# Performance work log

Measured on AMD Instinct MI355X. Metric: run time of the kernel, lower is better.

Reference implementation:

```python
import jax, jax.numpy as jnp
import numpy as np

# Model dims (match init_kwargs)
N_HEADS = 32
N_KV_HEADS = 8
DIM = 4096
HEAD_DIM = DIM // N_HEADS  # 128
N_REP = N_HEADS // N_KV_HEADS  # 4
MAX_SEQ_LEN = 2048
THETA = 10000.0


def precompute_freqs(dim, end, theta=THETA):
    inv = 1.0 / (theta ** (jnp.arange(0, dim, 2, dtype=jnp.float32) / dim))  # [dim/2]
    t = jnp.arange(end, dtype=jnp.float32)
    f = jnp.outer(t, inv)  # [end, dim/2]
    return jnp.cos(f), jnp.sin(f)


def apply_rope(x, cos, sin):
    # x: [b, s, h, d]; cos/sin: [s, d/2]. Pairs (x[...,2i], x[...,2i+1]) form complex numbers.
    xr = x[..., 0::2]
    xi = x[..., 1::2]
    c = cos[None, :, None, :]
    s = sin[None, :, None, :]
    out_r = xr * c - xi * s
    out_i = xr * s + xi * c
    return jnp.stack([out_r, out_i], axis=-1).reshape(x.shape)


def setup_inputs() -> dict:
    key = jax.random.key(0)
    ks = jax.random.split(key, 5)
    B, S = 4, 1024
    x = jax.random.normal(ks[0], (B, S, DIM), dtype=jnp.float32)
    wq = jax.random.normal(ks[1], (DIM, N_HEADS * HEAD_DIM), dtype=jnp.float32) * 0.02
    wk = jax.random.normal(ks[2], (DIM, N_KV_HEADS * HEAD_DIM), dtype=jnp.float32) * 0.02
    wv = jax.random.normal(ks[3], (DIM, N_KV_HEADS * HEAD_DIM), dtype=jnp.float32) * 0.02
    wo = jax.random.normal(ks[4], (N_HEADS * HEAD_DIM, DIM), dtype=jnp.float32) * 0.02
    # causal mask, additive: 0 on/below diagonal, -1e9 above
    mask = jnp.where(jnp.tril(jnp.ones((S, S), dtype=bool)), 0.0, -1e9).astype(jnp.float32)[None, None]
    return {"x": x, "wq": wq, "wk": wk, "wv": wv, "wo": wo, "mask": mask, "start_pos": 0}


def reference(x, wq, wk, wv, wo, mask, start_pos):
    B, S, _ = x.shape
    # QKV projections
    xq = (x @ wq).reshape(B, S, N_HEADS, HEAD_DIM)
    xk = (x @ wk).reshape(B, S, N_KV_HEADS, HEAD_DIM)
    xv = (x @ wv).reshape(B, S, N_KV_HEADS, HEAD_DIM)
    # RoPE on q, k at positions [start_pos, start_pos+S)
    cos, sin = precompute_freqs(HEAD_DIM, MAX_SEQ_LEN * 2)
    cos_s = jax.lax.dynamic_slice_in_dim(cos, start_pos, S, 0)
    sin_s = jax.lax.dynamic_slice_in_dim(sin, start_pos, S, 0)
    xq = apply_rope(xq, cos_s, sin_s)
    xk = apply_rope(xk, cos_s, sin_s)
    # KV-cache scatter-update (cache starts zeroed), then read prefix
    cache_k = jnp.zeros((B, MAX_SEQ_LEN, N_KV_HEADS, HEAD_DIM), dtype=x.dtype)
    cache_v = jnp.zeros_like(cache_k)
    cache_k = jax.lax.dynamic_update_slice(cache_k, xk, (0, start_pos, 0, 0))
    cache_v = jax.lax.dynamic_update_slice(cache_v, xv, (0, start_pos, 0, 0))
    kv_len = start_pos + S
    keys = cache_k[:, :kv_len]    # [b, kv_len, n_kv, d]
    values = cache_v[:, :kv_len]
    # GQA without materializing repeated KV: split q heads into (kv_group, rep)
    q = xq.reshape(B, S, N_KV_HEADS, N_REP, HEAD_DIM)
    scale = 1.0 / jnp.sqrt(jnp.float32(HEAD_DIM)).astype(x.dtype)
    scores = jnp.einsum('bsgrd,btgd->bgrst', q, keys) * scale  # [b, g, r, s, t]
    scores = scores + mask.reshape(1, 1, 1, S, kv_len)
    probs = jax.nn.softmax(scores, axis=-1)
    out = jnp.einsum('bgrst,btgd->bsgrd', probs, values)  # [b, s, g, r, d]
    out = out.reshape(B, S, N_HEADS * HEAD_DIM)
    return out @ wo
```

## Files before the change

kernel.cpp:

```cpp
#include <hip/hip_runtime.h>
#include <hip/hip_bf16.h>
#include <stdint.h>

typedef __bf16 bf16raw;
typedef __attribute__((ext_vector_type(8))) __bf16 bf16x8;
typedef __attribute__((ext_vector_type(4))) float f32x4;

#define DIMD 4096
#define NHEAD 32
#define NKVH 8
#define HD 128
#define SEQ 1024
#define NB 4
#define NTOK 4096
#define NQKV 6144

__device__ __forceinline__ void gload_lds16(const void* gsrc, void* ldst) {
  __builtin_amdgcn_global_load_lds(
      (const __attribute__((address_space(1))) void*)gsrc,
      (__attribute__((address_space(3))) void*)ldst, 16, 0, 0);
}

__global__ void cast_f32_bf16_kernel(const float* __restrict__ src,
                                     __hip_bfloat16* __restrict__ dst, int n) {
  int i = (blockIdx.x * 256 + threadIdx.x) * 8;
  if (i >= n) return;
  f32x4 a = *(const f32x4*)(src + i);
  f32x4 b = *(const f32x4*)(src + i + 4);
  union { bf16x8 v; __hip_bfloat16 e[8]; } o;
#pragma unroll
  for (int j = 0; j < 4; ++j) {
    o.e[j] = __float2bfloat16(a[j]);
    o.e[4 + j] = __float2bfloat16(b[j]);
  }
  *(bf16x8*)(dst + i) = o.v;
}

__global__ void transpose_cast_kernel(const float* __restrict__ src,
                                      __hip_bfloat16* __restrict__ dst,
                                      int K, int N) {
  __shared__ float tile[32][33];
  int n0 = blockIdx.x * 32, k0 = blockIdx.y * 32;
  int tx = threadIdx.x, ty = threadIdx.y;
#pragma unroll
  for (int i = 0; i < 4; ++i)
    tile[ty + 8 * i][tx] = src[(size_t)(k0 + ty + 8 * i) * N + n0 + tx];
  __syncthreads();
#pragma unroll
  for (int i = 0; i < 4; ++i)
    dst[(size_t)(n0 + ty + 8 * i) * K + k0 + tx] =
        __float2bfloat16(tile[tx][ty + 8 * i]);
}

__global__ void rope_table_kernel(float* __restrict__ cosb, float* __restrict__ sinb) {
  int idx = blockIdx.x * 256 + threadIdx.x;
  int s = idx >> 6, j = idx & 63;
  float inv = 1.0f / powf(10000.0f, (float)(2 * j) * (1.0f / 128.0f));
  float ang = (float)s * inv;
  cosb[idx] = cosf(ang);
  sinb[idx] = sinf(ang);
}

__global__ void v_transpose_kernel(const __hip_bfloat16* __restrict__ qkv,
                                   __hip_bfloat16* __restrict__ vt) {
  __shared__ __hip_bfloat16 tile[32][33];
  int bh = blockIdx.x;
  int s0 = blockIdx.y * 32;
  int d0 = blockIdx.z * 32;
  int b = bh >> 3, h = bh & 7;
  int tx = threadIdx.x, ty = threadIdx.y;
  const __hip_bfloat16* src =
      qkv + (size_t)(b * SEQ) * NQKV + DIMD + NKVH * HD + h * HD;
#pragma unroll
  for (int i = 0; i < 4; ++i)
    tile[ty + 8 * i][tx] = src[(size_t)(s0 + ty + 8 * i) * NQKV + d0 + tx];
  __syncthreads();
  int tIdx = s0 >> 6;
  int sLow = s0 & 32;
  __hip_bfloat16* dst = vt + ((size_t)bh * 16 + tIdx) * (128 * 64);
#pragma unroll
  for (int i = 0; i < 4; ++i)
    dst[(size_t)(d0 + ty + 8 * i) * 64 + sLow + tx] = tile[tx][ty + 8 * i];
}


#define LGSB()                                       \
  asm volatile("s_waitcnt lgkmcnt(0)" ::: "memory"); \
  __builtin_amdgcn_sched_barrier(0)

#define QMFMA(AFR, BFR, MB, NB)                                            \
  _Pragma("unroll") for (int mf2 = 0; mf2 < 4; ++mf2)                      \
  _Pragma("unroll") for (int nf2 = 0; nf2 < 2; ++nf2)                      \
  _Pragma("unroll") for (int kk2 = 0; kk2 < 2; ++kk2)                      \
      acc[(MB) + mf2][(NB) + nf2] = __builtin_amdgcn_mfma_f32_16x16x32_bf16( \
          AFR[mf2 * 2 + kk2], BFR[nf2 * 2 + kk2], acc[(MB) + mf2][(NB) + nf2], 0, 0, 0)

#define TILE4(BUF, ST1, ST2, ST3, ST4, VM)                        \
  {                                                               \
    _Pragma("unroll") for (int mf = 0; mf < 4; ++mf)              \
    _Pragma("unroll") for (int kk = 0; kk < 2; ++kk)              \
        alo[mf * 2 + kk] = ldsA(BUF, mf, kk);                     \
    _Pragma("unroll") for (int nf = 0; nf < 2; ++nf)              \
    _Pragma("unroll") for (int kk = 0; kk < 2; ++kk)              \
        bq[nf * 2 + kk] = ldsB(BUF, nf, kk);                      \
    ST1;                                                          \
    LGSB();                                                       \
    __builtin_amdgcn_s_setprio(1);                                \
    QMFMA(alo, bq, 0, 0);                                         \
    __builtin_amdgcn_s_setprio(0);                                \
    _Pragma("unroll") for (int mf = 0; mf < 4; ++mf)              \
    _Pragma("unroll") for (int kk = 0; kk < 2; ++kk)              \
        ahi[mf * 2 + kk] = ldsA(BUF, mf + 4, kk);                 \
    ST2;                                                          \
    LGSB();                                                       \
    __builtin_amdgcn_s_setprio(1);                                \
    QMFMA(ahi, bq, 4, 0);                                         \
    __builtin_amdgcn_s_setprio(0);                                \
    _Pragma("unroll") for (int nf = 0; nf < 2; ++nf)              \
    _Pragma("unroll") for (int kk = 0; kk < 2; ++kk)              \
        bq[nf * 2 + kk] = ldsB(BUF, nf + 2, kk);                  \
    LGSB();                                                       \
    __builtin_amdgcn_s_setprio(1);                                \
    QMFMA(alo, bq, 0, 2);                                         \
    __builtin_amdgcn_s_setprio(0);                                \
    __builtin_amdgcn_s_barrier();   \
    ST3;                                                          \
    ST4;                                                          \
    __builtin_amdgcn_s_setprio(1);                                \
    QMFMA(ahi, bq, 4, 2);                                         \
    __builtin_amdgcn_s_setprio(0);                                \
    VM;                                                           \
    __builtin_amdgcn_s_barrier();   \
  }

template <typename OutT, bool ROPE>
__global__ __launch_bounds__(512, 2) void gemm256_kernel(
    const __hip_bfloat16* __restrict__ A, const __hip_bfloat16* __restrict__ BT,
    OutT* __restrict__ C, int M, int N, int K,
    const float* __restrict__ cosb, const float* __restrict__ sinb) {
  __shared__ __align__(16) char lds_[131072];
  const int tid = threadIdx.x;
  const int w = tid >> 6, l = tid & 63;
  const int lr = l & 15, lk = l >> 4;
  const int wm = w >> 2, wn = w & 3;

  const int nbn = N >> 8;
  const int nwg = (M >> 8) * nbn;
  const int cpx = nwg >> 3;
  const int bid = blockIdx.x;
  const int swz = (bid & 7) * cpx + (bid >> 3);
  const int m0 = (swz / nbn) << 8;
  const int n0 = (swz % nbn) << 8;

  const size_t Kb = (size_t)K * 2;
  const char* Ab = (const char*)A + (size_t)m0 * Kb;
  const char* Bb = (const char*)BT + (size_t)n0 * Kb;
  const int srcb = ((l & 7) ^ (l >> 3)) * 16;
  const int crow = l >> 3;

  auto stageA = [&](int buf, int half, int kt) {
#pragma unroll
    for (int j = 0; j < 2; ++j) {
      int row = half * 128 + (w * 2 + j) * 8 + crow;
      gload_lds16(Ab + (size_t)row * Kb + (size_t)kt * 128 + srcb,
                  lds_ + buf * 65536 + half * 16384 + (w * 2 + j) * 1024);
    }
  };
  auto stageB = [&](int buf, int half, int kt) {
#pragma unroll
    for (int j = 0; j < 2; ++j) {
      int row = half * 128 + (w * 2 + j) * 8 + crow;
      gload_lds16(Bb + (size_t)row * Kb + (size_t)kt * 128 + srcb,
                  lds_ + buf * 65536 + 32768 + half * 16384 + (w * 2 + j) * 1024);
    }
  };
  auto ldsA = [&](int buf, int mf, int kk) {
    int rih = mf * 16 + lr;
    int cb = (kk * 64 + lk * 16) ^ ((lr & 7) << 4);
    return *(const bf16x8*)(lds_ + buf * 65536 + wm * 16384 + rih * 128 + cb);
  };
  auto ldsB = [&](int buf, int nf, int kk) {
    int rih = (wn & 1) * 64 + nf * 16 + lr;
    int cb = (kk * 64 + lk * 16) ^ ((lr & 7) << 4);
    return *(const bf16x8*)(lds_ + buf * 65536 + 32768 + (wn >> 1) * 16384 +
                            rih * 128 + cb);
  };

  f32x4 acc[8][4] = {};
  bf16x8 alo[8], ahi[8], bq[4];

  stageA(0, 0, 0);
  stageA(0, 1, 0);
  stageB(0, 0, 0);
  stageB(0, 1, 0);
  stageA(1, 0, 1);
  stageA(1, 1, 1);
  asm volatile("s_waitcnt vmcnt(4)" ::: "memory");
  __builtin_amdgcn_s_barrier();

  const int NT = K >> 6;
  for (int E = 0; E < NT - 2; E += 2) {
    TILE4(0, stageB(1, 0, E + 1), stageB(1, 1, E + 1),
          stageA(0, 0, E + 2), stageA(0, 1, E + 2),
          asm volatile("s_waitcnt vmcnt(4)" ::: "memory"));
    TILE4(1, stageB(0, 0, E + 2), stageB(0, 1, E + 2),
          stageA(1, 0, E + 3), stageA(1, 1, E + 3),
          asm volatile("s_waitcnt vmcnt(4)" ::: "memory"));
  }
  TILE4(0, stageB(1, 0, NT - 1), stageB(1, 1, NT - 1), (void)0, (void)0,
        asm volatile("s_waitcnt vmcnt(0)" ::: "memory"));
  TILE4(1, (void)0, (void)0, (void)0, (void)0, (void)0);

#pragma unroll
  for (int mf = 0; mf < 8; ++mf) {
    int row = m0 + wm * 128 + mf * 16 + lk * 4;
#pragma unroll
    for (int nf = 0; nf < 4; ++nf) {
      int colb = n0 + wn * 64 + nf * 16;
      f32x4 v = acc[mf][nf];
      if constexpr (ROPE) {
        if (colb < 5120) {
          int d = (colb & 127) + lr;
          int jj = d >> 1;
          bool even = (d & 1) == 0;
#pragma unroll
          for (int j = 0; j < 4; ++j) {
            float p = __shfl_xor(v[j], 1);
            int s = (row + j) & (SEQ - 1);
            float c = cosb[s * 64 + jj];
            float sn = sinb[s * 64 + jj];
            v[j] = even ? (v[j] * c - p * sn) : (p * sn + v[j] * c);
          }
        }
      }
#pragma unroll
      for (int j = 0; j < 4; ++j) {
        size_t off = (size_t)(row + j) * N + colb + lr;
        if constexpr (sizeof(OutT) == 2)
          C[off] = __float2bfloat16(v[j]);
        else
          C[off] = v[j];
      }
    }
  }
}

__global__ __launch_bounds__(256, 2) void attn_kernel(
    const __hip_bfloat16* __restrict__ qkv,
    const __hip_bfloat16* __restrict__ vtc,
    __hip_bfloat16* __restrict__ out) {
  __shared__ __align__(16) char Ks[2][16384];
  __shared__ __align__(16) char Vs[2][16384];
  __shared__ __align__(16) char Ps[4][2048];

  const int tid = threadIdx.x;
  const int w = tid >> 6, l = tid & 63;
  const int lr = l & 15, lk = l >> 4;
  const int bx = blockIdx.x;
  const int pair = bx >> 7;
  const int hb = bx & 127;
  const int h = hb & 31;
  const int b = hb >> 5;
  const int hk = h >> 2;

  const char* KgB = (const char*)qkv +
                    ((size_t)(b * SEQ) * NQKV + DIMD + hk * HD) * 2;
  const char* VgB = (const char*)vtc + (size_t)(b * NKVH + hk) * (16 * 16384);
  char* Pw = &Ps[w][0];

  const float cs = 0.12752039889171495f;
  const float ebias = 11.541560327111707f;

  auto stageK = [&](int buf, int kvb) {
#pragma unroll
    for (int j = 0; j < 4; ++j) {
      int i = w * 4 + j;
      int row = i * 4 + (l >> 4);
      int si = ((l & 15) * 16) ^ ((row & 7) << 4);
      gload_lds16(KgB + (size_t)(kvb + row) * (NQKV * 2) + si,
                  &Ks[buf][i * 1024]);
    }
  };
  auto stageV = [&](int buf, int t) {
#pragma unroll
    for (int j = 0; j < 4; ++j) {
      int i = w * 4 + j;
      int row = i * 8 + (l >> 3);
      int si = ((l & 7) * 16) ^ ((row & 7) << 4);
      gload_lds16(VgB + (size_t)t * 16384 + row * 128 + si,
                  &Vs[buf][i * 1024]);
    }
  };

  for (int qsel = 0; qsel < 2; ++qsel) {
    const int qtile = qsel ? (15 - pair) : pair;
    const int qbase = qtile * 64 + w * 16;
    const int nkv = qtile + 1;

    const __hip_bfloat16* Qp =
        qkv + (size_t)(b * SEQ + qbase + lr) * NQKV + h * HD + lk * 8;
    bf16x8 aq[4];
#pragma unroll
    for (int ks = 0; ks < 4; ++ks) aq[ks] = *(const bf16x8*)(Qp + ks * 32);

    f32x4 O[8] = {};
    float lsum[4] = {0.f, 0.f, 0.f, 0.f};

    stageK(0, 0);
    stageV(0, 0);
    asm volatile("s_waitcnt vmcnt(0)" ::: "memory");
    __syncthreads();

    for (int t = 0; t < nkv; ++t) {
      const int cur = t & 1;
      if (t + 1 < nkv) {
        stageK(cur ^ 1, (t + 1) * 64);
        stageV(cur ^ 1, t + 1);
      }
      const int kvb = t * 64;

      f32x4 st[4] = {};
      __builtin_amdgcn_s_setprio(1);
#pragma unroll
      for (int nt = 0; nt < 4; ++nt) {
        int row = nt * 16 + lr;
        const char* kr = &Ks[cur][row * 256];
        int sw = (row & 7) << 4;
#pragma unroll
        for (int ks = 0; ks < 4; ++ks) {
          bf16x8 bk = *(const bf16x8*)(kr + ((ks * 64 + lk * 16) ^ sw));
          st[nt] = __builtin_amdgcn_mfma_f32_16x16x32_bf16(aq[ks], bk, st[nt], 0, 0, 0);
        }
      }
      __builtin_amdgcn_s_setprio(0);

      const bool needmask = (kvb + 63 > qbase);
#pragma unroll
      for (int j = 0; j < 4; ++j) {
        int qrow = qbase + lk * 4 + j;
        int prow = lk * 4 + j;
        int sw = (prow & 7) << 4;
#pragma unroll
        for (int nt = 0; nt < 4; ++nt) {
          float p = exp2f(fmaf(st[nt][j], cs, -ebias));
          if (needmask && (kvb + nt * 16 + lr > qrow)) p = 0.f;
          lsum[j] += p;
          *(__hip_bfloat16*)(Pw + prow * 128 + (((nt * 16 + lr) * 2) ^ sw)) =
              __float2bfloat16(p);
        }
      }

      asm volatile("s_waitcnt lgkmcnt(0)" ::: "memory");
      __builtin_amdgcn_sched_barrier(0);

      __builtin_amdgcn_s_setprio(1);
#pragma unroll
      for (int ks = 0; ks < 2; ++ks) {
        bf16x8 ap = *(const bf16x8*)(Pw + lr * 128 +
                                     ((ks * 64 + lk * 16) ^ ((lr & 7) << 4)));
#pragma unroll
        for (int dt = 0; dt < 8; ++dt) {
          int row = dt * 16 + lr;
          bf16x8 bv = *(const bf16x8*)(&Vs[cur][row * 128 +
                                               ((ks * 64 + lk * 16) ^ ((row & 7) << 4))]);
          O[dt] = __builtin_amdgcn_mfma_f32_16x16x32_bf16(ap, bv, O[dt], 0, 0, 0);
        }
      }
      __builtin_amdgcn_s_setprio(0);

      __syncthreads();
    }

#pragma unroll
    for (int j = 0; j < 4; ++j) {
      float rs = lsum[j];
      rs += __shfl_xor(rs, 1);
      rs += __shfl_xor(rs, 2);
      rs += __shfl_xor(rs, 4);
      rs += __shfl_xor(rs, 8);
      float inv = 1.0f / rs;
      __hip_bfloat16* orow =
          out + (size_t)(b * SEQ + qbase + lk * 4 + j) * DIMD + h * HD;
#pragma unroll
      for (int dt = 0; dt < 8; ++dt)
        orow[dt * 16 + lr] = __float2bfloat16(O[dt][j] * inv);
    }
  }
}

extern "C" void kernel_launch(void* const* d_in, const int* in_sizes, int n_in,
                              void* d_out, int out_size, void* d_ws, size_t ws_size,
                              hipStream_t stream) {
  const float* x = (const float*)d_in[0];
  const float* wq = (const float*)d_in[1];
  const float* wk = (const float*)d_in[2];
  const float* wv = (const float*)d_in[3];
  const float* wo = (const float*)d_in[4];
  float* out = (float*)d_out;

  char* ws = (char*)d_ws;
  const size_t MB = 1024 * 1024;
  __hip_bfloat16* xb = (__hip_bfloat16*)(ws);
  __hip_bfloat16* wqkvt = (__hip_bfloat16*)(ws + 32 * MB);
  __hip_bfloat16* wot = (__hip_bfloat16*)(ws + 80 * MB);
  __hip_bfloat16* qkv = (__hip_bfloat16*)(ws + 112 * MB);
  __hip_bfloat16* vtc = (__hip_bfloat16*)(ws + 160 * MB);
  float* cosb = (float*)(ws + 168 * MB);
  float* sinb = cosb + SEQ * 64;

  cast_f32_bf16_kernel<<<NTOK * DIMD / 8 / 256, 256, 0, stream>>>(x, xb, NTOK * DIMD);
  transpose_cast_kernel<<<dim3(128, 128), dim3(32, 8), 0, stream>>>(wq, wqkvt, 4096, 4096);
  transpose_cast_kernel<<<dim3(32, 128), dim3(32, 8), 0, stream>>>(
      wk, wqkvt + (size_t)4096 * 4096, 4096, 1024);
  transpose_cast_kernel<<<dim3(32, 128), dim3(32, 8), 0, stream>>>(
      wv, wqkvt + (size_t)5120 * 4096, 4096, 1024);
  transpose_cast_kernel<<<dim3(128, 128), dim3(32, 8), 0, stream>>>(wo, wot, 4096, 4096);
  rope_table_kernel<<<SEQ * 64 / 256, 256, 0, stream>>>(cosb, sinb);
  gemm256_kernel<__hip_bfloat16, true><<<dim3(384), 512, 0, stream>>>(
      xb, wqkvt, qkv, NTOK, NQKV, DIMD, cosb, sinb);
  v_transpose_kernel<<<dim3(32, 32, 4), dim3(32, 8), 0, stream>>>(qkv, vtc);
  attn_kernel<<<dim3(1024), 256, 0, stream>>>(qkv, vtc, xb);
  gemm256_kernel<float, false><<<dim3(256), 512, 0, stream>>>(
      xb, wot, out, NTOK, DIMD, DIMD, nullptr, nullptr);
}
```

Measured before the change: 482.4 us.

## Use 16 waves per GEMM block with 64x64 per-wave tiles

Restructures the 256x256 bf16 GEMM to run with 1024 threads (16 waves in a 4x4 grid), so each wave computes a 64x64 sub-tile instead of 128x64. This halves the per-wave accumulator and fragment registers. Staging is simplified so each wave loads 16 rows of A and B per tile, and the inner schedule becomes a two-phase MFMA loop with one barrier and prefetch per k-tile. The aim is more waves to hide latency, at the cost of more LDS reads per MFMA and more barrier synchronisation across 16 waves. The launch_bounds of (1024,4) appears inconsistent with 128KB of LDS per block.

```diff
diff --git a/kernel.cpp b/kernel.cpp
--- a/kernel.cpp
+++ b/kernel.cpp
@@ -88,53 +88,40 @@
   asm volatile("s_waitcnt lgkmcnt(0)" ::: "memory"); \
   __builtin_amdgcn_sched_barrier(0)
 
-#define QMFMA(AFR, BFR, MB, NB)                                            \
+#define HMFMA(NB)                                                          \
   _Pragma("unroll") for (int mf2 = 0; mf2 < 4; ++mf2)                      \
   _Pragma("unroll") for (int nf2 = 0; nf2 < 2; ++nf2)                      \
   _Pragma("unroll") for (int kk2 = 0; kk2 < 2; ++kk2)                      \
-      acc[(MB) + mf2][(NB) + nf2] = __builtin_amdgcn_mfma_f32_16x16x32_bf16( \
-          AFR[mf2 * 2 + kk2], BFR[nf2 * 2 + kk2], acc[(MB) + mf2][(NB) + nf2], 0, 0, 0)
-
-#define TILE4(BUF, ST1, ST2, ST3, ST4, VM)                        \
+      acc[mf2][(NB) + nf2] = __builtin_amdgcn_mfma_f32_16x16x32_bf16(      \
+          af[mf2 * 2 + kk2], bq[nf2 * 2 + kk2], acc[mf2][(NB) + nf2], 0, 0, 0)
+
+#define TILE(BUF, KT2, DOSTAGE, VMN)                              \
   {                                                               \
     _Pragma("unroll") for (int mf = 0; mf < 4; ++mf)              \
     _Pragma("unroll") for (int kk = 0; kk < 2; ++kk)              \
-        alo[mf * 2 + kk] = ldsA(BUF, mf, kk);                     \
+        af[mf * 2 + kk] = ldsA(BUF, mf, kk);                      \
     _Pragma("unroll") for (int nf = 0; nf < 2; ++nf)              \
     _Pragma("unroll") for (int kk = 0; kk < 2; ++kk)              \
         bq[nf * 2 + kk] = ldsB(BUF, nf, kk);                      \
-    ST1;                                                          \
     LGSB();                                                       \
     __builtin_amdgcn_s_setprio(1);                                \
-    QMFMA(alo, bq, 0, 0);                                         \
-    __builtin_amdgcn_s_setprio(0);                                \
-    _Pragma("unroll") for (int mf = 0; mf < 4; ++mf)              \
-    _Pragma("unroll") for (int kk = 0; kk < 2; ++kk)              \
-        ahi[mf * 2 + kk] = ldsA(BUF, mf + 4, kk);                 \
-    ST2;                                                          \
-    LGSB();                                                       \
-    __builtin_amdgcn_s_setprio(1);                                \
-    QMFMA(ahi, bq, 4, 0);                                         \
+    HMFMA(0);                                                     \
     __builtin_amdgcn_s_setprio(0);                                \
     _Pragma("unroll") for (int nf = 0; nf < 2; ++nf)              \
     _Pragma("unroll") for (int kk = 0; kk < 2; ++kk)              \
         bq[nf * 2 + kk] = ldsB(BUF, nf + 2, kk);                  \
     LGSB();                                                       \
+    __builtin_amdgcn_s_barrier();      \
+    if (DOSTAGE) { stageA(BUF, KT2); stageB(BUF, KT2); }          \
     __builtin_amdgcn_s_setprio(1);                                \
-    QMFMA(alo, bq, 0, 2);                                         \
+    HMFMA(2);                                                     \
     __builtin_amdgcn_s_setprio(0);                                \
-    __builtin_amdgcn_s_barrier();   \
-    ST3;                                                          \
-    ST4;                                                          \
-    __builtin_amdgcn_s_setprio(1);                                \
-    QMFMA(ahi, bq, 4, 2);                                         \
-    __builtin_amdgcn_s_setprio(0);                                \
-    VM;                                                           \
-    __builtin_amdgcn_s_barrier();   \
+    asm volatile("s_waitcnt vmcnt(" #VMN ")" ::: "memory");       \
+    __builtin_amdgcn_s_barrier();        \
   }
 
 template <typename OutT, bool ROPE>
-__global__ __launch_bounds__(512, 2) void gemm256_kernel(
+__global__ __launch_bounds__(1024, 4) void gemm256_kernel(
     const __hip_bfloat16* __restrict__ A, const __hip_bfloat16* __restrict__ BT,
     OutT* __restrict__ C, int M, int N, int K,
     const float* __restrict__ cosb, const float* __restrict__ sinb) {
@@ -156,64 +143,56 @@
   const char* Ab = (const char*)A + (size_t)m0 * Kb;
   const char* Bb = (const char*)BT + (size_t)n0 * Kb;
   const int srcb = ((l & 7) ^ (l >> 3)) * 16;
-  const int crow = l >> 3;
-
-  auto stageA = [&](int buf, int half, int kt) {
+  const int srow = l >> 3;
+
+  auto stageA = [&](int buf, int kt) {
 #pragma unroll
     for (int j = 0; j < 2; ++j) {
-      int row = half * 128 + (w * 2 + j) * 8 + crow;
+      int row = w * 16 + j * 8 + srow;
       gload_lds16(Ab + (size_t)row * Kb + (size_t)kt * 128 + srcb,
-                  lds_ + buf * 65536 + half * 16384 + (w * 2 + j) * 1024);
-    }
-  };
-  auto stageB = [&](int buf, int half, int kt) {
+                  lds_ + buf * 65536 + (w * 16 + j * 8) * 128);
+    }
+  };
+  auto stageB = [&](int buf, int kt) {
 #pragma unroll
     for (int j = 0; j < 2; ++j) {
-      int row = half * 128 + (w * 2 + j) * 8 + crow;
+      int row = w * 16 + j * 8 + srow;
       gload_lds16(Bb + (size_t)row * Kb + (size_t)kt * 128 + srcb,
-                  lds_ + buf * 65536 + 32768 + half * 16384 + (w * 2 + j) * 1024);
+                  lds_ + buf * 65536 + 32768 + (w * 16 + j * 8) * 128);
     }
   };
   auto ldsA = [&](int buf, int mf, int kk) {
-    int rih = mf * 16 + lr;
+    int rih = wm * 64 + mf * 16 + lr;
     int cb = (kk * 64 + lk * 16) ^ ((lr & 7) << 4);
-    return *(const bf16x8*)(lds_ + buf * 65536 + wm * 16384 + rih * 128 + cb);
+    return *(const bf16x8*)(lds_ + buf * 65536 + rih * 128 + cb);
   };
   auto ldsB = [&](int buf, int nf, int kk) {
-    int rih = (wn & 1) * 64 + nf * 16 + lr;
+    int rih = wn * 64 + nf * 16 + lr;
     int cb = (kk * 64 + lk * 16) ^ ((lr & 7) << 4);
-    return *(const bf16x8*)(lds_ + buf * 65536 + 32768 + (wn >> 1) * 16384 +
-                            rih * 128 + cb);
-  };
-
-  f32x4 acc[8][4] = {};
-  bf16x8 alo[8], ahi[8], bq[4];
-
-  stageA(0, 0, 0);
-  stageA(0, 1, 0);
-  stageB(0, 0, 0);
-  stageB(0, 1, 0);
-  stageA(1, 0, 1);
-  stageA(1, 1, 1);
+    return *(const bf16x8*)(lds_ + buf * 65536 + 32768 + rih * 128 + cb);
+  };
+
+  f32x4 acc[4][4] = {};
+  bf16x8 af[8], bq[4];
+
+  stageA(0, 0);
+  stageB(0, 0);
+  stageA(1, 1);
+  stageB(1, 1);
   asm volatile("s_waitcnt vmcnt(4)" ::: "memory");
   __builtin_amdgcn_s_barrier();
 
   const int NT = K >> 6;
   for (int E = 0; E < NT - 2; E += 2) {
-    TILE4(0, stageB(1, 0, E + 1), stageB(1, 1, E + 1),
-          stageA(0, 0, E + 2), stageA(0, 1, E + 2),
-          asm volatile("s_waitcnt vmcnt(4)" ::: "memory"));
-    TILE4(1, stageB(0, 0, E + 2), stageB(0, 1, E + 2),
-          stageA(1, 0, E + 3), stageA(1, 1, E + 3),
-          asm volatile("s_waitcnt vmcnt(4)" ::: "memory"));
+    TILE(0, E + 2, true, 4);
+    TILE(1, E + 3, true, 4);
   }
-  TILE4(0, stageB(1, 0, NT - 1), stageB(1, 1, NT - 1), (void)0, (void)0,
-        asm volatile("s_waitcnt vmcnt(0)" ::: "memory"));
-  TILE4(1, (void)0, (void)0, (void)0, (void)0, (void)0);
-
-#pragma unroll
-  for (int mf = 0; mf < 8; ++mf) {
-    int row = m0 + wm * 128 + mf * 16 + lk * 4;
+  TILE(0, 0, false, 0);
+  TILE(1, 0, false, 0);
+
+#pragma unroll
+  for (int mf = 0; mf < 4; ++mf) {
+    int row = m0 + wm * 64 + mf * 16 + lk * 4;
 #pragma unroll
     for (int nf = 0; nf < 4; ++nf) {
       int colb = n0 + wn * 64 + nf * 16;
@@ -416,10 +395,10 @@
       wv, wqkvt + (size_t)5120 * 4096, 4096, 1024);
   transpose_cast_kernel<<<dim3(128, 128), dim3(32, 8), 0, stream>>>(wo, wot, 4096, 4096);
   rope_table_kernel<<<SEQ * 64 / 256, 256, 0, stream>>>(cosb, sinb);
-  gemm256_kernel<__hip_bfloat16, true><<<dim3(384), 512, 0, stream>>>(
+  gemm256_kernel<__hip_bfloat16, true><<<dim3(384), 1024, 0, stream>>>(
       xb, wqkvt, qkv, NTOK, NQKV, DIMD, cosb, sinb);
   v_transpose_kernel<<<dim3(32, 32, 4), dim3(32, 8), 0, stream>>>(qkv, vtc);
   attn_kernel<<<dim3(1024), 256, 0, stream>>>(qkv, vtc, xb);
-  gemm256_kernel<float, false><<<dim3(256), 512, 0, stream>>>(
+  gemm256_kernel<float, false><<<dim3(256), 1024, 0, stream>>>(
       xb, wot, out, NTOK, DIMD, DIMD, nullptr, nullptr);
 }
```

Result: slower. 1.404 ms (+190.9%).
